# Kernel optimization log

Hardware: AMD Instinct MI355X
Metric: run time of the kernel (lower is better)

Reference implementation:

```python
import jax, jax.numpy as jnp
import numpy as np

EPS = 1e-8

def _cosine_sim(a, b):
    # a: [B,Nq,D], b: [B,Np,D] -> [B,Nq,Np]
    an = a / (jnp.linalg.norm(a, axis=-1, keepdims=True) + EPS)
    bn = b / (jnp.linalg.norm(b, axis=-1, keepdims=True) + EPS)
    return jnp.einsum('bqd,bpd->bqp', an, bn)

def _sq_dist(a, b):
    # squared euclidean pairwise distance: [B,Nq,Np]
    d = (jnp.sum(a * a, -1)[:, :, None] + jnp.sum(b * b, -1)[:, None, :]
         - 2.0 * jnp.einsum('bqd,bpd->bqp', a, b))
    return jnp.maximum(d, 0.0)

def setup_inputs() -> dict:
    key = jax.random.key(0)
    ks = jax.random.split(key, 6)
    B, N, D, H = 8, 2048, 256, 16
    return {
        'f1': jax.random.normal(ks[0], (B, N, D), jnp.float32),
        'f2': jax.random.normal(ks[1], (B, N, D), jnp.float32),
        'p': jax.random.normal(ks[2], (B, N, 3), jnp.float32),
        'q': jax.random.normal(ks[3], (B, N, 3), jnp.float32),
        'W1': jax.random.normal(ks[4], (H, 2), jnp.float32) * 0.5,
        'b1': jnp.zeros((H,), jnp.float32),
        'W2': jax.random.normal(ks[5], (1, H), jnp.float32) * 0.5,
        'b2': jnp.zeros((1,), jnp.float32),
        'similar_num': 8,
    }

def reference(f1, f2, p, q, W1, b1, W2, b2, similar_num):
    B, Nq, _ = q.shape
    Np = p.shape[1]
    # pairwise similarities
    w1 = _cosine_sim(f2, f1)            # [B,Nq,Np] feature cosine sim
    w2 = -_sq_dist(q, p)                # [B,Nq,Np] negative coord distance
    # similar_net: pointwise MLP over channel dim (2 -> H -> 1)
    w_in = jnp.stack([w1.reshape(B, -1), w2.reshape(B, -1)], axis=1)  # [B,2,L]
    h = jax.nn.relu(jnp.einsum('bcl,hc->bhl', w_in, W1) + b1[None, :, None])
    w = (jnp.einsum('bhl,oh->bol', h, W2) + b2[None, :, None]).reshape(B, Nq, Np)
    # get_weighted_similarity: topk + softmax-weighted pooling + max pooling
    vals, idx = jax.lax.top_k(w, similar_num)          # [B,Nq,k] (sorted desc, as torch.topk)
    ws = jax.nn.softmax(vals, axis=-1)                 # softmax over gathered scores
    feat = jax.vmap(lambda z, i: z[i])(f1, idx)        # [B,Nq,k,D] gather
    feat_max = jnp.max(feat, axis=2)                   # [B,Nq,D]
    feat_w = jnp.einsum('bqk,bqkd->bqd', ws, feat)     # [B,Nq,D]
    f = jnp.concatenate([feat_w, feat_max], axis=-1)   # [B,Nq,2D]
    return f, idx, w
```

## Files before the change

### kernel.cpp

```cpp
#include <hip/hip_runtime.h>
#include <math.h>

constexpr int B_ = 8;
constexpr int N_ = 2048;
constexpr int D_ = 256;
constexpr int H_ = 16;
constexpr int K_ = 8;
constexpr int POOL = 64;
constexpr int PSEL = 24;

constexpr int BM = 128;
constexpr int BK = 32;

typedef _Float16 f16x8 __attribute__((ext_vector_type(8)));
typedef float    f32x4 __attribute__((ext_vector_type(4)));
typedef float    f32x2 __attribute__((ext_vector_type(2)));

typedef __attribute__((address_space(3))) unsigned int       lds_u32_t;
typedef __attribute__((address_space(1))) const unsigned int glb_u32_t;

__device__ __forceinline__ void g2l16(const void* g, void* l) {
    __builtin_amdgcn_global_load_lds((glb_u32_t*)g, (lds_u32_t*)l, 16, 0, 0);
}

__device__ __forceinline__ unsigned ford(float f) {
    unsigned u = __float_as_uint(f);
    return (u & 0x80000000u) ? ~u : (u | 0x80000000u);
}
__device__ __forceinline__ float unford(unsigned t) {
    return (t & 0x80000000u) ? __uint_as_float(t & 0x7FFFFFFFu)
                             : __uint_as_float(~t);
}

__device__ __forceinline__ unsigned pk16(_Float16 a, _Float16 b) {
    unsigned short ua = __builtin_bit_cast(unsigned short, a);
    unsigned short ub = __builtin_bit_cast(unsigned short, b);
    return (unsigned)ua | ((unsigned)ub << 16);
}

__device__ inline void split4_f16(float4 v, float s, uint2& hi, uint2& lo) {
    float a = v.x * s, b = v.y * s, c = v.z * s, d = v.w * s;
    _Float16 ha = (_Float16)a, hb = (_Float16)b;
    _Float16 hc = (_Float16)c, hd = (_Float16)d;
    _Float16 la = (_Float16)(a - (float)ha), lb = (_Float16)(b - (float)hb);
    _Float16 lc = (_Float16)(c - (float)hc), ld = (_Float16)(d - (float)hd);
    hi.x = pk16(ha, hb); hi.y = pk16(hc, hd);
    lo.x = pk16(la, lb); lo.y = pk16(lc, ld);
}

__global__ __launch_bounds__(256)
void prep_kernel(const float* __restrict__ f1, const float* __restrict__ f2,
                 unsigned short* __restrict__ s1h, unsigned short* __restrict__ s1l,
                 unsigned short* __restrict__ s2h, double* __restrict__ dinv1) {
    int gid  = blockIdx.x * blockDim.x + threadIdx.x;
    int wave = gid >> 6;
    int lane = gid & 63;
    if (wave >= 2 * B_ * N_) return;
    bool is1 = wave < B_ * N_;
    int r = is1 ? wave : wave - B_ * N_;

    const float* src = (is1 ? f1 : f2) + (size_t)r * D_;
    float4 v = *(const float4*)(src + lane * 4);
    float ss = v.x * v.x + v.y * v.y + v.z * v.z + v.w * v.w;
#pragma unroll
    for (int off = 32; off > 0; off >>= 1) ss += __shfl_xor(ss, off, 64);
    float inv = 1.0f / (sqrtf(ss) + 1e-8f);

    uint2 hi, lo;
    split4_f16(v, inv, hi, lo);

    int panel = r >> 7, rloc = r & 127;
    int s     = lane >> 1;
    int chunk = s >> 2;
    int sl    = (s & 3) ^ ((rloc >> 1) & 3);
    int half  = lane & 1;
    size_t idx = ((size_t)(panel * 8 + chunk) << 12)
               + (size_t)rloc * 32 + sl * 8 + half * 4;
    if (is1) {
        *(uint2*)&s1h[idx] = hi;
        *(uint2*)&s1l[idx] = lo;
        double dss = (double)v.x * v.x + (double)v.y * v.y
                   + (double)v.z * v.z + (double)v.w * v.w;
#pragma unroll
        for (int off = 32; off > 0; off >>= 1) dss += __shfl_xor(dss, off, 64);
        if (lane == 0) dinv1[r] = 1.0 / (sqrt(dss) + 1e-8);
    } else {
        *(uint2*)&s2h[idx] = hi;
    }
}

__global__ __launch_bounds__(256, 3)
void gemm_mlp_kernel(const unsigned short* __restrict__ aH0,
                     const unsigned short* __restrict__ bH0,
                     const unsigned short* __restrict__ bL0,
                     const float* __restrict__ pc, const float* __restrict__ qc,
                     const float* __restrict__ pW1, const float* __restrict__ pb1,
                     const float* __restrict__ pW2, const float* __restrict__ pb2,
                     float* __restrict__ w_out) {
    __shared__ unsigned short ldsbuf[2 * 3 * 4096];

    int tid = threadIdx.x;
    int l  = blockIdx.x + (blockIdx.y << 4);
    int ls = ((l & 7) << 5) | (l >> 3);
    int pBase = (ls & 15) * BM;
    int qBase = (ls >> 4) * BM;
    int b = blockIdx.z;

    int lane = tid & 63;
    int wv   = tid >> 6;
    int wq = (wv >> 1) * 64;
    int wp = (wv & 1) * 64;
    int fr = lane & 15;
    int kg = lane >> 4;

    const int Apanel8 = ((b * N_ + qBase) >> 7) * 8;
    const int Bpanel8 = ((b * N_ + pBase) >> 7) * 8;

    char* ldsB = (char*)&ldsbuf[0];
    const int wlo = (wv << 11) + (lane << 4);
    const int wdo = (wv << 11);
    const int cw  = (kg ^ ((fr >> 1) & 3)) << 4;

    f32x4 acc[4][4] = {};

#define STAGE(buf, c)                                                          \
    {                                                                          \
        const char* aH = (const char*)aH0 + ((size_t)(Apanel8 + (c)) << 13);   \
        const char* bH = (const char*)bH0 + ((size_t)(Bpanel8 + (c)) << 13);   \
        const char* bL = (const char*)bL0 + ((size_t)(Bpanel8 + (c)) << 13);   \
        char* dst = ldsB + (buf) * 24576;                                      \
        _Pragma("unroll")                                                      \
        for (int i = 0; i < 2; i++) {                                          \
            int o = i << 10;                                                   \
            g2l16(aH + wlo + o, dst + 0     + wdo + o);                        \
            g2l16(bH + wlo + o, dst + 8192  + wdo + o);                        \
            g2l16(bL + wlo + o, dst + 16384 + wdo + o);                        \
        }                                                                      \
    }

    STAGE(0, 0);
    __syncthreads();

#pragma unroll
    for (int c = 0; c < 8; c++) {
        if (c < 7) STAGE((c + 1) & 1, c + 1);

        char* base = ldsB + (c & 1) * 24576;
        f16x8 ah[4], bh[4], bl[4];
#pragma unroll
        for (int t = 0; t < 4; t++) {
            int ra = (wq + t * 16 + fr) * 64;
            int rb = (wp + t * 16 + fr) * 64;
            ah[t] = *(const f16x8*)(base + 0     + ra + cw);
            bh[t] = *(const f16x8*)(base + 8192  + rb + cw);
            bl[t] = *(const f16x8*)(base + 16384 + rb + cw);
        }
#pragma unroll
        for (int qt = 0; qt < 4; qt++) {
#pragma unroll
            for (int pt = 0; pt < 4; pt++) {
                acc[qt][pt] = __builtin_amdgcn_mfma_f32_16x16x32_f16(
                    ah[qt], bh[pt], acc[qt][pt], 0, 0, 0);
                acc[qt][pt] = __builtin_amdgcn_mfma_f32_16x16x32_f16(
                    ah[qt], bl[pt], acc[qt][pt], 0, 0, 0);
            }
        }
        __syncthreads();
    }
#undef STAGE

    float Wa[H_], Wb[H_], Bb[H_], Wo[H_];
#pragma unroll
    for (int h = 0; h < H_; h++) {
        Wa[h] = pW1[2 * h]; Wb[h] = pW1[2 * h + 1];
        Bb[h] = pb1[h];     Wo[h] = pW2[h];
    }
    float base2 = pb2[0];

    float px[4], py[4], pz[4], pn2[4];
    int pg[4];
#pragma unroll
    for (int pt = 0; pt < 4; pt++) {
        int p = pBase + wp + pt * 16 + fr;
        pg[pt] = p;
        const float* pp = pc + ((size_t)(b * N_ + p)) * 3;
        px[pt] = pp[0]; py[pt] = pp[1]; pz[pt] = pp[2];
        pn2[pt] = px[pt] * px[pt] + py[pt] * py[pt] + pz[pt] * pz[pt];
    }
#pragma unroll
    for (int qt = 0; qt < 4; qt++) {
        float qx[4], qy[4], qz[4], qq2[4];
        int q0 = qBase + wq + qt * 16 + kg * 4;
#pragma unroll
        for (int r = 0; r < 4; r++) {
            const float* qp = qc + ((size_t)(b * N_ + q0 + r)) * 3;
            qx[r] = qp[0]; qy[r] = qp[1]; qz[r] = qp[2];
            qq2[r] = qx[r] * qx[r] + qy[r] * qy[r] + qz[r] * qz[r];
        }
#pragma unroll
        for (int pt = 0; pt < 4; pt++) {
            f32x4 cval = acc[qt][pt];
            float w2v[4];
#pragma unroll
            for (int r = 0; r < 4; r++) {
                float d2 = qq2[r] + pn2[pt]
                         - 2.f * (qx[r] * px[pt] + qy[r] * py[pt] + qz[r] * pz[pt]);
                w2v[r] = -fmaxf(d2, 0.f);
            }
#pragma unroll
            for (int pr = 0; pr < 2; pr++) {
                f32x2 w1p = { cval[2 * pr], cval[2 * pr + 1] };
                f32x2 w2p = { w2v[2 * pr], w2v[2 * pr + 1] };
                f32x2 outp = { base2, base2 };
#pragma unroll
                for (int h = 0; h < H_; h++) {
                    f32x2 t = w1p * Wa[h] + w2p * Wb[h] + Bb[h];
                    t = __builtin_elementwise_max(t, (f32x2){0.f, 0.f});
                    outp += Wo[h] * t;
                }
                w_out[((size_t)(b * N_ + q0 + 2 * pr)) * N_ + pg[pt]]     = outp.x;
                w_out[((size_t)(b * N_ + q0 + 2 * pr + 1)) * N_ + pg[pt]] = outp.y;
            }
        }
    }
}

__global__ __launch_bounds__(256)
void topk_kernel(const float* __restrict__ w, const float* __restrict__ f1,
                 const float* __restrict__ f2,
                 const float* __restrict__ pc, const float* __restrict__ qc,
                 const float* __restrict__ pW1, const float* __restrict__ pb1,
                 const float* __restrict__ pW2, const float* __restrict__ pb2,
                 const double* __restrict__ dinv1,
                 float* __restrict__ f_out, float* __restrict__ idx_out) {
    __shared__ int    s_cand[4][POOL];
    __shared__ double s_val[4][POOL];
    __shared__ int    s_idx[4][POOL];
    __shared__ double s_rv[4][K_];
    __shared__ int    s_ri[4][K_];

    int tid  = threadIdx.x;
    int wix  = tid >> 6;
    int lane = tid & 63;
    int row  = blockIdx.x * 4 + wix;
    int b    = row >> 11;
    const float* wrow = w + (size_t)row * N_;

    float4 v4s[8];
    float mymax = -INFINITY;
#pragma unroll
    for (int j = 0; j < 8; j++) {
        v4s[j] = *(const float4*)(wrow + lane * 4 + j * 256);
        mymax = fmaxf(mymax,
                 fmaxf(fmaxf(v4s[j].x, v4s[j].y), fmaxf(v4s[j].z, v4s[j].w)));
    }

    unsigned mk = ford(mymax);
    unsigned T = 0;
    for (int bit = 31; bit >= 0; --bit) {
        unsigned c = T | (1u << bit);
        if (__popcll(__ballot(mk >= c)) >= PSEL) T = c;
    }
    float Tf = unford(T);

    unsigned long long below = (1ull << lane) - 1ull;
    int total = 0;
#pragma unroll
    for (int j = 0; j < 8; j++) {
        float vv[4] = {v4s[j].x, v4s[j].y, v4s[j].z, v4s[j].w};
#pragma unroll
        for (int c = 0; c < 4; c++) {
            bool in = vv[c] >= Tf;
            unsigned long long m = __ballot(in);
            if (in) {
                int pos = total + __popcll(m & below);
                if (pos < POOL) s_cand[wix][pos] = lane * 4 + j * 256 + c;
            }
            total += __popcll(m);
        }
    }
    int ncand = total < POOL ? total : POOL;
    asm volatile("s_waitcnt lgkmcnt(0)" ::: "memory");

    int sl = lane & 7;
    int gr = lane >> 3;
    const float* f2r = f2 + (size_t)row * D_ + sl * 32;
    float4 a4[8];
#pragma unroll
    for (int t = 0; t < 8; t++) a4[t] = *(const float4*)(f2r + t * 4);

    double daa = 0.0;
#pragma unroll
    for (int t = 0; t < 8; t++) {
        daa += (double)a4[t].x * (double)a4[t].x;
        daa += (double)a4[t].y * (double)a4[t].y;
        daa += (double)a4[t].z * (double)a4[t].z;
        daa += (double)a4[t].w * (double)a4[t].w;
    }
#pragma unroll
    for (int off = 1; off < 8; off <<= 1) daa += __shfl_xor(daa, off, 64);
    double inv_a = 1.0 / (sqrt(daa) + 1e-8);

    double mydab = 0.0;
    int myci = 0;
    int NR = (ncand + 7) >> 3;
    for (int r = 0; r < NR; r++) {
        int k = 8 * r + gr;
        int cj = (k < ncand) ? s_cand[wix][k] : 0;
        const float* f1r = f1 + ((size_t)(b * N_ + cj)) * D_ + sl * 32;
        double sA = 0.0;
#pragma unroll
        for (int t = 0; t < 8; t++) {
            float4 b4 = *(const float4*)(f1r + t * 4);
            sA += (double)a4[t].x * (double)b4.x;
            sA += (double)a4[t].y * (double)b4.y;
            sA += (double)a4[t].z * (double)b4.z;
            sA += (double)a4[t].w * (double)b4.w;
        }
#pragma unroll
        for (int off = 1; off < 8; off <<= 1) sA += __shfl_xor(sA, off, 64);
        if (sl == r) { mydab = sA; myci = cj; }
    }

    int myk = 8 * sl + gr;
    double ex = -INFINITY;
    int    ei = 0x7fffffff;
    if (myk < ncand) {
        ei = myci;
        double w1d = mydab * inv_a * dinv1[b * N_ + myci];
        const float* qp = qc + (size_t)row * 3;
        double qx = qp[0], qy = qp[1], qz = qp[2];
        const float* pp = pc + ((size_t)(b * N_ + myci)) * 3;
        double px = pp[0], py = pp[1], pz = pp[2];
        double d2 = (qx * qx + qy * qy + qz * qz) + (px * px + py * py + pz * pz)
                  - 2.0 * (qx * px + qy * py + qz * pz);
        double w2d = -fmax(d2, 0.0);
        double out = (double)pb2[0];
#pragma unroll
        for (int h = 0; h < H_; h++) {
            double t = (double)pW1[2 * h] * w1d + (double)pW1[2 * h + 1] * w2d
                     + (double)pb1[h];
            out += (double)pW2[h] * fmax(t, 0.0);
        }
        ex = out;
    }

    s_val[wix][myk] = ex;
    s_idx[wix][myk] = ei;
    asm volatile("s_waitcnt lgkmcnt(0)" ::: "memory");
    {
        int rank = 0;
#pragma unroll
        for (int j = 0; j < POOL; j++) {
            double vj = s_val[wix][j];
            int    ij = s_idx[wix][j];
            rank += (vj > ex || (vj == ex && ij < ei)) ? 1 : 0;
        }
        if (rank < K_) { s_rv[wix][rank] = ex; s_ri[wix][rank] = ei; }
    }
    asm volatile("s_waitcnt lgkmcnt(0)" ::: "memory");

    double outv[K_];
    int    outi[K_];
#pragma unroll
    for (int r = 0; r < K_; r++) { outv[r] = s_rv[wix][r]; outi[r] = s_ri[wix][r]; }

    float m = (float)outv[0];
    float e[K_], s = 0.f;
#pragma unroll
    for (int r = 0; r < K_; r++) { e[r] = expf((float)outv[r] - m); s += e[r]; }
    float inv_s = 1.f / s;

    const float* f1b = f1 + ((size_t)b * N_) * D_;
    size_t obase = (size_t)row * (2 * D_);
#pragma unroll
    for (int jd = 0; jd < D_ / 64; jd++) {
        int d = lane + 64 * jd;
        float accv = 0.f, mx = -INFINITY;
#pragma unroll
        for (int r = 0; r < K_; r++) {
            float x = f1b[(size_t)outi[r] * D_ + d];
            accv += (e[r] * inv_s) * x;
            mx = fmaxf(mx, x);
        }
        f_out[obase + d]      = accv;
        f_out[obase + D_ + d] = mx;
    }
    if (lane == 0) {
#pragma unroll
        for (int r = 0; r < K_; r++) idx_out[(size_t)row * K_ + r] = (float)outi[r];
    }
}

extern "C" void kernel_launch(void* const* d_in, const int* in_sizes, int n_in,
                              void* d_out, int out_size, void* d_ws, size_t ws_size,
                              hipStream_t stream) {
    const float* f1 = (const float*)d_in[0];
    const float* f2 = (const float*)d_in[1];
    const float* pc = (const float*)d_in[2];
    const float* qc = (const float*)d_in[3];
    const float* W1 = (const float*)d_in[4];
    const float* b1 = (const float*)d_in[5];
    const float* W2 = (const float*)d_in[6];
    const float* b2 = (const float*)d_in[7];

    float* out     = (float*)d_out;
    float* f_out   = out;
    float* idx_out = f_out + (size_t)B_ * N_ * 2 * D_;
    float* w_out   = idx_out + (size_t)B_ * N_ * K_;

    unsigned short* s1h = (unsigned short*)f_out;
    unsigned short* s1l = s1h + (size_t)B_ * N_ * D_;
    unsigned short* s2h = s1l + (size_t)B_ * N_ * D_;

    double* dinv1 = (double*)d_ws;

    prep_kernel<<<(2 * B_ * N_) / 4, 256, 0, stream>>>(f1, f2, s1h, s1l, s2h,
                                                       dinv1);

    dim3 g2(N_ / BM, N_ / BM, B_);
    gemm_mlp_kernel<<<g2, 256, 0, stream>>>(s2h, s1h, s1l, pc, qc,
                                            W1, b1, W2, b2, w_out);

    topk_kernel<<<(B_ * N_) / 4, 256, 0, stream>>>(w_out, f1, f2, pc, qc,
                                                   W1, b1, W2, b2, dinv1,
                                                   f_out, idx_out);
}
```

Baseline: 388.3 us.

## Compute coordinate distance via MFMA on augmented split-f16 vectors and pack MLP pairs

Coordinates are packed into 32-wide augmented f16 vectors (scaled hi/lo split plus negative norms and ones) in the prep kernel. The epilogue then gets the negative squared distance from one MFMA per tile instead of scalar FMA math per element. The MLP loop is restructured to process hidden units in pairs with packed FMAs, and each element is written individually. This removes scalar distance arithmetic and coordinate loads from the GEMM epilogue, at the cost of f16-split precision in the distance term and extra scratch writes of the augmented vectors.

```diff
diff --git a/kernel.cpp b/kernel.cpp
--- a/kernel.cpp
+++ b/kernel.cpp
@@ -50,8 +50,11 @@
 
 __global__ __launch_bounds__(256)
 void prep_kernel(const float* __restrict__ f1, const float* __restrict__ f2,
+                 const float* __restrict__ pcoord, const float* __restrict__ qcoord,
                  unsigned short* __restrict__ s1h, unsigned short* __restrict__ s1l,
-                 unsigned short* __restrict__ s2h, double* __restrict__ dinv1) {
+                 unsigned short* __restrict__ s2h,
+                 unsigned short* __restrict__ qaug, unsigned short* __restrict__ paug,
+                 double* __restrict__ dinv1) {
     int gid  = blockIdx.x * blockDim.x + threadIdx.x;
     int wave = gid >> 6;
     int lane = gid & 63;
@@ -87,13 +90,49 @@
     } else {
         *(uint2*)&s2h[idx] = hi;
     }
+
+    if (lane == 0) {
+        const float* cp = (is1 ? pcoord : qcoord) + (size_t)r * 3;
+        float x = cp[0], y = cp[1], z = cp[2];
+        const float s2 = 1.41421356237309515f;
+        _Float16 xh = (_Float16)(s2 * x), yh = (_Float16)(s2 * y), zh = (_Float16)(s2 * z);
+        _Float16 xl = (_Float16)(s2 * x - (float)xh);
+        _Float16 yl = (_Float16)(s2 * y - (float)yh);
+        _Float16 zl = (_Float16)(s2 * z - (float)zh);
+        float nn = x * x + y * y + z * z;
+        _Float16 nh = (_Float16)nn, nl = (_Float16)(nn - (float)nh);
+        _Float16 one = (_Float16)1.0f;
+        _Float16 mnh = -nh, mnl = -nl;
+        unsigned short h[32];
+#pragma unroll
+        for (int i = 0; i < 32; i++) h[i] = 0;
+#define US_(v) __builtin_bit_cast(unsigned short, v)
+        if (is1) {
+            h[0] = US_(xh); h[1] = US_(yh); h[2] = US_(zh);
+            h[3] = US_(xh); h[4] = US_(yh); h[5] = US_(zh);
+            h[6] = US_(xl); h[7] = US_(yl); h[8] = US_(zl);
+            h[9] = US_(one); h[10] = US_(one);
+            h[11] = US_(mnh); h[12] = US_(mnl);
+        } else {
+            h[0] = US_(xh); h[1] = US_(yh); h[2] = US_(zh);
+            h[3] = US_(xl); h[4] = US_(yl); h[5] = US_(zl);
+            h[6] = US_(xh); h[7] = US_(yh); h[8] = US_(zh);
+            h[9] = US_(mnh); h[10] = US_(mnl);
+            h[11] = US_(one); h[12] = US_(one);
+        }
+#undef US_
+        unsigned short* dst = (is1 ? paug : qaug) + (size_t)r * 32;
+#pragma unroll
+        for (int i = 0; i < 4; i++) ((uint4*)dst)[i] = ((const uint4*)h)[i];
+    }
 }
 
 __global__ __launch_bounds__(256, 3)
 void gemm_mlp_kernel(const unsigned short* __restrict__ aH0,
                      const unsigned short* __restrict__ bH0,
                      const unsigned short* __restrict__ bL0,
-                     const float* __restrict__ pc, const float* __restrict__ qc,
+                     const unsigned short* __restrict__ qaug,
+                     const unsigned short* __restrict__ paug,
                      const float* __restrict__ pW1, const float* __restrict__ pb1,
                      const float* __restrict__ pW2, const float* __restrict__ pb2,
                      float* __restrict__ w_out) {
@@ -169,57 +208,44 @@
     }
 #undef STAGE
 
-    float Wa[H_], Wb[H_], Bb[H_], Wo[H_];
-#pragma unroll
-    for (int h = 0; h < H_; h++) {
-        Wa[h] = pW1[2 * h]; Wb[h] = pW1[2 * h + 1];
-        Bb[h] = pb1[h];     Wo[h] = pW2[h];
-    }
-    float base2 = pb2[0];
-
-    float px[4], py[4], pz[4], pn2[4];
-    int pg[4];
-#pragma unroll
-    for (int pt = 0; pt < 4; pt++) {
-        int p = pBase + wp + pt * 16 + fr;
-        pg[pt] = p;
-        const float* pp = pc + ((size_t)(b * N_ + p)) * 3;
-        px[pt] = pp[0]; py[pt] = pp[1]; pz[pt] = pp[2];
-        pn2[pt] = px[pt] * px[pt] + py[pt] * py[pt] + pz[pt] * pz[pt];
-    }
+    f32x2 Wap[8], Wbp[8], Bbp[8], Wop[8];
+#pragma unroll
+    for (int hp = 0; hp < 8; hp++) {
+        Wap[hp] = (f32x2){pW1[4 * hp],     pW1[4 * hp + 2]};
+        Wbp[hp] = (f32x2){pW1[4 * hp + 1], pW1[4 * hp + 3]};
+        Bbp[hp] = (f32x2){pb1[2 * hp],     pb1[2 * hp + 1]};
+        Wop[hp] = (f32x2){pW2[2 * hp],     pW2[2 * hp + 1]};
+    }
+    float b2v = pb2[0];
+
+    const unsigned short* qa_base = qaug + ((size_t)(b * N_ + qBase + wq) << 5) + kg * 8;
+    const unsigned short* pa_base = paug + ((size_t)(b * N_ + pBase + wp) << 5) + kg * 8;
+
 #pragma unroll
     for (int qt = 0; qt < 4; qt++) {
-        float qx[4], qy[4], qz[4], qq2[4];
-        int q0 = qBase + wq + qt * 16 + kg * 4;
-#pragma unroll
-        for (int r = 0; r < 4; r++) {
-            const float* qp = qc + ((size_t)(b * N_ + q0 + r)) * 3;
-            qx[r] = qp[0]; qy[r] = qp[1]; qz[r] = qp[2];
-            qq2[r] = qx[r] * qx[r] + qy[r] * qy[r] + qz[r] * qz[r];
-        }
+        f16x8 aaug = *(const f16x8*)(qa_base + ((qt * 16 + fr) << 5));
+        int rowb = qBase + wq + qt * 16 + kg * 4;
 #pragma unroll
         for (int pt = 0; pt < 4; pt++) {
+            f16x8 baug = *(const f16x8*)(pa_base + ((pt * 16 + fr) << 5));
+            f32x4 sacc = __builtin_amdgcn_mfma_f32_16x16x32_f16(
+                aaug, baug, (f32x4){0.f, 0.f, 0.f, 0.f}, 0, 0, 0);
             f32x4 cval = acc[qt][pt];
-            float w2v[4];
+            int col = pBase + wp + pt * 16 + fr;
 #pragma unroll
             for (int r = 0; r < 4; r++) {
-                float d2 = qq2[r] + pn2[pt]
-                         - 2.f * (qx[r] * px[pt] + qy[r] * py[pt] + qz[r] * pz[pt]);
-                w2v[r] = -fmaxf(d2, 0.f);
-            }
-#pragma unroll
-            for (int pr = 0; pr < 2; pr++) {
-                f32x2 w1p = { cval[2 * pr], cval[2 * pr + 1] };
-                f32x2 w2p = { w2v[2 * pr], w2v[2 * pr + 1] };
-                f32x2 outp = { base2, base2 };
-#pragma unroll
-                for (int h = 0; h < H_; h++) {
-                    f32x2 t = w1p * Wa[h] + w2p * Wb[h] + Bb[h];
+                float w1 = cval[r];
+                float w2 = fminf(sacc[r], 0.f);
+                f32x2 w1p = {w1, w1}, w2p = {w2, w2};
+                f32x2 o = {b2v, 0.f};
+#pragma unroll
+                for (int hp = 0; hp < 8; hp++) {
+                    f32x2 t = __builtin_elementwise_fma(w2p, Wbp[hp], Bbp[hp]);
+                    t = __builtin_elementwise_fma(w1p, Wap[hp], t);
                     t = __builtin_elementwise_max(t, (f32x2){0.f, 0.f});
-                    outp += Wo[h] * t;
+                    o = __builtin_elementwise_fma(t, Wop[hp], o);
                 }
-                w_out[((size_t)(b * N_ + q0 + 2 * pr)) * N_ + pg[pt]]     = outp.x;
-                w_out[((size_t)(b * N_ + q0 + 2 * pr + 1)) * N_ + pg[pt]] = outp.y;
+                w_out[((size_t)(b * N_ + rowb + r)) * N_ + col] = o.x + o.y;
             }
         }
     }
@@ -409,17 +435,20 @@
     float* idx_out = f_out + (size_t)B_ * N_ * 2 * D_;
     float* w_out   = idx_out + (size_t)B_ * N_ * K_;
 
-    unsigned short* s1h = (unsigned short*)f_out;
-    unsigned short* s1l = s1h + (size_t)B_ * N_ * D_;
-    unsigned short* s2h = s1l + (size_t)B_ * N_ * D_;
+    unsigned short* s1h  = (unsigned short*)f_out;
+    unsigned short* s1l  = s1h + (size_t)B_ * N_ * D_;
+    unsigned short* s2h  = s1l + (size_t)B_ * N_ * D_;
+    unsigned short* qaug = s2h + (size_t)B_ * N_ * D_;
+    unsigned short* paug = qaug + (size_t)B_ * N_ * 32;
 
     double* dinv1 = (double*)d_ws;
 
-    prep_kernel<<<(2 * B_ * N_) / 4, 256, 0, stream>>>(f1, f2, s1h, s1l, s2h,
-                                                       dinv1);
+    prep_kernel<<<(2 * B_ * N_) / 4, 256, 0, stream>>>(f1, f2, pc, qc,
+                                                       s1h, s1l, s2h,
+                                                       qaug, paug, dinv1);
 
     dim3 g2(N_ / BM, N_ / BM, B_);
-    gemm_mlp_kernel<<<g2, 256, 0, stream>>>(s2h, s1h, s1l, pc, qc,
+    gemm_mlp_kernel<<<g2, 256, 0, stream>>>(s2h, s1h, s1l, qaug, paug,
                                             W1, b1, W2, b2, w_out);
 
     topk_kernel<<<(B_ * N_) / 4, 256, 0, stream>>>(w_out, f1, f2, pc, qc,
```

After: 379.0 us. 2.4% less time.
